# Kernel tuning notes

Measured on AMD Instinct MI355X. Metric: run time of the kernel, lower is better.

Reference implementation:

```python
import jax, jax.numpy as jnp
import numpy as np
from jax.scipy.linalg import expm

B, Z_DIM, MAT_DIM = 131072, 512, 10
INIT_SCALE = 0.001


def setup_inputs() -> dict:
    key = jax.random.key(0)
    k_z, k_basis = jax.random.split(key)
    z = jax.random.normal(k_z, (B, Z_DIM), dtype=jnp.float32)
    # nn.Parameter ~ Normal(0, lie_alg_init_scale)
    lie_alg_basis = INIT_SCALE * jax.random.normal(k_basis, (Z_DIM, MAT_DIM, MAT_DIM), dtype=jnp.float32)
    return {"z": z, "lie_alg_basis": lie_alg_basis}


def reference(z, lie_alg_basis):
    # lie_alg[b] = sum_z z[b,z] * basis[z]  -- single batched contraction
    lie_alg = jnp.einsum('bz,zij->bij', z, lie_alg_basis)  # [B, mat_dim, mat_dim]
    # batched matrix exponential over tiny 10x10 matrices
    lie_group = jax.vmap(expm)(lie_alg)
    return lie_group
```

## Files before the change

### kernel.cpp

```cpp
#include <hip/hip_runtime.h>

#define B_TOTAL 131072
#define KDIM    512
#define NDIM    100
#define NPAD    112
#define NT      7
#define NTERMS  7

using bf16x8 = __attribute__((ext_vector_type(8))) short;
using f32x4  = __attribute__((ext_vector_type(4))) float;

__device__ __forceinline__ unsigned short f2bf(float x) {
    union { float f; unsigned u; } v; v.f = x;
    unsigned r = v.u + 0x7fffu + ((v.u >> 16) & 1u);
    return (unsigned short)(r >> 16);
}

__global__ __launch_bounds__(256) void basis_prep_kernel(
    const float* __restrict__ basis, unsigned short* __restrict__ btT)
{
    const int idx = blockIdx.x * 256 + threadIdx.x;
    const int n = idx >> 9;
    const int k = idx & 511;
    btT[idx] = (n < NDIM) ? f2bf(basis[(size_t)k * NDIM + n]) : (unsigned short)0;
}

__global__ __launch_bounds__(256) void lie_gemm_direct(
    const float* __restrict__ z, const unsigned short* __restrict__ btT,
    float* __restrict__ out)
{
    const int t    = threadIdx.x;
    const int wave = t >> 6;
    const int lane = t & 63;
    const int ln   = lane & 15;
    const int kq   = (lane >> 4) * 8;
    const int m0   = blockIdx.x * 128 + wave * 32;

    const float* zr0 = &z[(size_t)(m0 + ln) * KDIM + kq];
    const float* zr1 = zr0 + (size_t)16 * KDIM;
    const unsigned short* bp = &btT[(size_t)ln * KDIM + kq];

    f32x4 acc[2][NT];
#pragma unroll
    for (int mt = 0; mt < 2; ++mt)
#pragma unroll
        for (int nt = 0; nt < NT; ++nt)
            acc[mt][nt] = (f32x4){0.f, 0.f, 0.f, 0.f};

#pragma unroll 1
    for (int ks = 0; ks < KDIM; ks += 32) {
        const float4 va0 = *(const float4*)&zr0[ks];
        const float4 va1 = *(const float4*)&zr0[ks + 4];
        const float4 vb0 = *(const float4*)&zr1[ks];
        const float4 vb1 = *(const float4*)&zr1[ks + 4];

        bf16x8 a0, a1;
        a0[0] = f2bf(va0.x); a0[1] = f2bf(va0.y); a0[2] = f2bf(va0.z); a0[3] = f2bf(va0.w);
        a0[4] = f2bf(va1.x); a0[5] = f2bf(va1.y); a0[6] = f2bf(va1.z); a0[7] = f2bf(va1.w);
        a1[0] = f2bf(vb0.x); a1[1] = f2bf(vb0.y); a1[2] = f2bf(vb0.z); a1[3] = f2bf(vb0.w);
        a1[4] = f2bf(vb1.x); a1[5] = f2bf(vb1.y); a1[6] = f2bf(vb1.z); a1[7] = f2bf(vb1.w);

#pragma unroll
        for (int nt = 0; nt < NT; ++nt) {
            const bf16x8 bf = *(const bf16x8*)&bp[(size_t)nt * 16 * KDIM + ks];
            acc[0][nt] = __builtin_amdgcn_mfma_f32_16x16x32_bf16(a0, bf, acc[0][nt], 0, 0, 0);
            acc[1][nt] = __builtin_amdgcn_mfma_f32_16x16x32_bf16(a1, bf, acc[1][nt], 0, 0, 0);
        }
    }

#pragma unroll
    for (int mt = 0; mt < 2; ++mt) {
        const int mbase = m0 + mt * 16 + ((lane >> 4) << 2);
#pragma unroll
        for (int nt = 0; nt < NT; ++nt) {
            const int n = nt * 16 + ln;
            if (n < NDIM) {
#pragma unroll
                for (int r = 0; r < 4; ++r)
                    out[(size_t)(mbase + r) * NDIM + n] = acc[mt][nt][r];
            }
        }
    }
}

__global__ __launch_bounds__(256, 2) void lie_expm_kernel(float* __restrict__ out)
{
    const int b = blockIdx.x * 256 + threadIdx.x;
    const size_t base = (size_t)b * NDIM;

    float A[100];
#pragma unroll
    for (int s = 0; s < 25; ++s) {
        const float4 v = *(const float4*)&out[base + s * 4];
        A[s * 4 + 0] = v.x;
        A[s * 4 + 1] = v.y;
        A[s * 4 + 2] = v.z;
        A[s * 4 + 3] = v.w;
    }

#pragma unroll 1
    for (int i = 0; i < 10; ++i) {
        float u[10];
#pragma unroll
        for (int j = 0; j < 10; ++j) u[j] = (j == i) ? 1.f : 0.f;

#pragma unroll 1
        for (int k = NTERMS; k >= 1; --k) {
            float tmp[10];
#pragma unroll
            for (int j = 0; j < 10; ++j) tmp[j] = 0.f;
#pragma unroll
            for (int m = 0; m < 10; ++m) {
                const float um = u[m];
#pragma unroll
                for (int j = 0; j < 10; ++j)
                    tmp[j] = fmaf(um, A[m * 10 + j], tmp[j]);
            }
            const float inv = 1.f / (float)k;
#pragma unroll
            for (int j = 0; j < 10; ++j)
                u[j] = ((j == i) ? 1.f : 0.f) + tmp[j] * inv;
        }

#pragma unroll
        for (int s = 0; s < 5; ++s) {
            float2 v;
            v.x = u[s * 2];
            v.y = u[s * 2 + 1];
            *(float2*)&out[base + (size_t)i * 10 + s * 2] = v;
        }
    }
}

extern "C" void kernel_launch(void* const* d_in, const int* in_sizes, int n_in,
                              void* d_out, int out_size, void* d_ws, size_t ws_size,
                              hipStream_t stream)
{
    const float* z     = (const float*)d_in[0];
    const float* basis = (const float*)d_in[1];
    float* out         = (float*)d_out;
    unsigned short* btT = (unsigned short*)d_ws;

    basis_prep_kernel<<<(NPAD * KDIM) / 256, 256, 0, stream>>>(basis, btT);
    lie_gemm_direct<<<B_TOTAL / 128, 256, 0, stream>>>(z, btT, out);
    lie_expm_kernel<<<B_TOTAL / 256, 256, 0, stream>>>(out);
}
```

Measured before the change: 426.0 us.

## Fuse GEMM and matrix exponential via LDS staging with two threads per matrix

Result: faster. 409.1 us (-4.0%).

```diff
diff --git a/kernel.cpp b/kernel.cpp
--- a/kernel.cpp
+++ b/kernel.cpp
@@ -6,6 +6,7 @@
 #define NPAD    112
 #define NT      7
 #define NTERMS  7
+#define LSTRIDE 108
 
 using bf16x8 = __attribute__((ext_vector_type(8))) short;
 using f32x4  = __attribute__((ext_vector_type(4))) float;
@@ -25,10 +26,12 @@
     btT[idx] = (n < NDIM) ? f2bf(basis[(size_t)k * NDIM + n]) : (unsigned short)0;
 }
 
-__global__ __launch_bounds__(256) void lie_gemm_direct(
+__global__ __launch_bounds__(256, 2) void lie_fused(
     const float* __restrict__ z, const unsigned short* __restrict__ btT,
     float* __restrict__ out)
 {
+    __shared__ __align__(16) float lds[128 * LSTRIDE];
+
     const int t    = threadIdx.x;
     const int wave = t >> 6;
     const int lane = t & 63;
@@ -68,43 +71,48 @@
         }
     }
 
+    const int lb0 = wave * 32 + ((lane >> 4) << 2);
 #pragma unroll
     for (int mt = 0; mt < 2; ++mt) {
-        const int mbase = m0 + mt * 16 + ((lane >> 4) << 2);
 #pragma unroll
         for (int nt = 0; nt < NT; ++nt) {
             const int n = nt * 16 + ln;
             if (n < NDIM) {
 #pragma unroll
                 for (int r = 0; r < 4; ++r)
-                    out[(size_t)(mbase + r) * NDIM + n] = acc[mt][nt][r];
+                    lds[(lb0 + mt * 16 + r) * LSTRIDE + n] = acc[mt][nt][r];
             }
         }
     }
-}
 
-__global__ __launch_bounds__(256, 2) void lie_expm_kernel(float* __restrict__ out)
-{
-    const int b = blockIdx.x * 256 + threadIdx.x;
-    const size_t base = (size_t)b * NDIM;
+    __syncthreads();
+
+    const int mb   = t >> 1;
+    const int tpar = t & 1;
+    const size_t gbase = ((size_t)blockIdx.x * 128 + mb) * NDIM;
 
     float A[100];
 #pragma unroll
     for (int s = 0; s < 25; ++s) {
-        const float4 v = *(const float4*)&out[base + s * 4];
-        A[s * 4 + 0] = v.x;
-        A[s * 4 + 1] = v.y;
-        A[s * 4 + 2] = v.z;
-        A[s * 4 + 3] = v.w;
+        const f32x4 v = *(const f32x4*)&lds[mb * LSTRIDE + s * 4];
+        A[s * 4 + 0] = v[0];
+        A[s * 4 + 1] = v[1];
+        A[s * 4 + 2] = v[2];
+        A[s * 4 + 3] = v[3];
     }
 
 #pragma unroll 1
-    for (int i = 0; i < 10; ++i) {
-        float u[10];
+    for (int ii = 0; ii < 5; ++ii) {
+        const int i = tpar * 5 + ii;
+
+        float e[10], u[10];
 #pragma unroll
-        for (int j = 0; j < 10; ++j) u[j] = (j == i) ? 1.f : 0.f;
+        for (int j = 0; j < 10; ++j) {
+            e[j] = (j == i) ? 1.f : 0.f;
+            u[j] = e[j];
+        }
 
-#pragma unroll 1
+#pragma unroll
         for (int k = NTERMS; k >= 1; --k) {
             float tmp[10];
 #pragma unroll
@@ -119,15 +127,15 @@
             const float inv = 1.f / (float)k;
 #pragma unroll
             for (int j = 0; j < 10; ++j)
-                u[j] = ((j == i) ? 1.f : 0.f) + tmp[j] * inv;
+                u[j] = fmaf(tmp[j], inv, e[j]);
         }
 
 #pragma unroll
         for (int s = 0; s < 5; ++s) {
-            float2 v;
-            v.x = u[s * 2];
-            v.y = u[s * 2 + 1];
-            *(float2*)&out[base + (size_t)i * 10 + s * 2] = v;
+            float2 v2;
+            v2.x = u[s * 2];
+            v2.y = u[s * 2 + 1];
+            *(float2*)&out[gbase + (size_t)i * 10 + s * 2] = v2;
         }
     }
 }
@@ -142,6 +150,5 @@
     unsigned short* btT = (unsigned short*)d_ws;
 
     basis_prep_kernel<<<(NPAD * KDIM) / 256, 256, 0, stream>>>(basis, btT);
-    lie_gemm_direct<<<B_TOTAL / 128, 256, 0, stream>>>(z, btT, out);
-    lie_expm_kernel<<<B_TOTAL / 256, 256, 0, stream>>>(out);
+    lie_fused<<<B_TOTAL / 128, 256, 0, stream>>>(z, btT, out);
 }
```
